# Performance work log

Hardware: AMD Instinct MI355X
Metric: run time of the kernel (lower is better)

The kernel has to match this reference:

```python
import jax, jax.numpy as jnp
import numpy as np

C = 32
C_Z = 128
S = 256   # MSA depth
N = 384   # residues


def setup_inputs() -> dict:
    key = jax.random.key(0)
    ks = jax.random.split(key, 7)
    m = jax.random.normal(ks[0], (S, N, C), dtype=jnp.float32)
    gamma = jnp.ones((C,), dtype=jnp.float32)
    beta = jnp.zeros((C,), dtype=jnp.float32)
    # projections stored as [in, out]
    W1 = jax.random.normal(ks[1], (C, C), dtype=jnp.float32) / np.sqrt(C)
    W2 = jax.random.normal(ks[2], (C, C), dtype=jnp.float32) / np.sqrt(C)
    W3 = jax.random.normal(ks[3], (C * C, C_Z), dtype=jnp.float32) / np.sqrt(C * C)
    b3 = jnp.zeros((C_Z,), dtype=jnp.float32)
    return {"m": m, "gamma": gamma, "beta": beta, "W1": W1, "W2": W2, "W3": W3, "b3": b3}


def reference(m, gamma, beta, W1, W2, W3, b3):
    # LayerNorm over channel dim
    mu = jnp.mean(m, axis=-1, keepdims=True)
    var = jnp.mean(jnp.square(m - mu), axis=-1, keepdims=True)
    mn = (m - mu) * jax.lax.rsqrt(var + 1e-5) * gamma + beta
    a = jnp.einsum('sic,cd->sid', mn, W1)  # [s, n, c]
    b = jnp.einsum('sic,cd->sid', mn, W2)  # [s, n, c]
    # outer product, mean over MSA dim s -> [n, n, c, c]
    o = jnp.einsum('sic,sjd->ijcd', a, b) / a.shape[0]
    o = o.reshape(o.shape[0], o.shape[1], C * C)  # [n, n, c*c]
    z = o @ W3 + b3  # [n, n, c_z]
    return z
```

## Files before the change

kernel.cpp:

```cpp
#include <hip/hip_runtime.h>

#define S_DEPTH 256
#define NRES 384
#define CIN 32
#define CZ 128
#define MDIM (NRES * CIN)

typedef short bf16x8 __attribute__((ext_vector_type(8)));
typedef short short4v __attribute__((ext_vector_type(4)));
typedef float f32x4 __attribute__((ext_vector_type(4)));

static __device__ __forceinline__ unsigned short f2bf(float f) {
  unsigned int u = __float_as_uint(f);
  unsigned int r = (u + 0x7fffu + ((u >> 16) & 1u)) >> 16;
  return (unsigned short)r;
}

static __device__ __forceinline__ void gld16(const void* g, void* l) {
  __builtin_amdgcn_global_load_lds((__attribute__((address_space(1))) void*)(g),
                                   (__attribute__((address_space(3))) void*)(l),
                                   16, 0, 0);
}

__global__ __launch_bounds__(256) void k_pre(
    const float* __restrict__ mm, const float* __restrict__ gamma,
    const float* __restrict__ beta, const float* __restrict__ W1,
    const float* __restrict__ W2, const float* __restrict__ W3,
    unsigned short* __restrict__ aT, unsigned short* __restrict__ bT,
    unsigned short* __restrict__ W3T) {
  __shared__ __align__(16) char sraw[256 * 33 * 4];
  const int t = threadIdx.x;

  if (blockIdx.x < 16) {
    unsigned short (*tile)[72] = (unsigned short(*)[72])sraw;
    const int b = blockIdx.x;
    const int d0 = (b & 7) * 4;
    const int e0 = (b >> 3) * 64;
#pragma unroll
    for (int iter = 0; iter < 32; ++iter) {
      int lr_ = iter * 4 + (t >> 6);
      int c = lr_ >> 2, dl = lr_ & 3;
      int q = c * 32 + d0 + dl;
      tile[lr_][t & 63] = f2bf(W3[q * 128 + e0 + (t & 63)]);
    }
    __syncthreads();
    const int e_l = t >> 2;
    const int dl = t & 3;
    unsigned short* dst = W3T + (((size_t)(d0 + dl) * 128) + e0 + e_l) * 32;
#pragma unroll
    for (int j = 0; j < 32; ++j) dst[j] = tile[j * 4 + dl][e_l];
    return;
  }

  float* buf = (float*)sraw;
  const int i = blockIdx.x - 16;

#pragma unroll
  for (int it = 0; it < 8; ++it) {
    int s = it * 32 + (t >> 3);
    int c4 = (t & 7) * 4;
    const float4 v = *(const float4*)(mm + ((size_t)s * NRES + i) * CIN + c4);
    buf[s * 33 + c4 + 0] = v.x;
    buf[s * 33 + c4 + 1] = v.y;
    buf[s * 33 + c4 + 2] = v.z;
    buf[s * 33 + c4 + 3] = v.w;
  }
  __syncthreads();

  float x[32];
#pragma unroll
  for (int k = 0; k < 32; ++k) x[k] = buf[t * 33 + k];
  float mu = 0.f;
#pragma unroll
  for (int k = 0; k < 32; ++k) mu += x[k];
  mu *= (1.f / 32.f);
  float var = 0.f;
#pragma unroll
  for (int k = 0; k < 32; ++k) {
    float dk = x[k] - mu;
    var += dk * dk;
  }
  var *= (1.f / 32.f);
  float inv = rsqrtf(var + 1e-5f);
#pragma unroll
  for (int k = 0; k < 32; ++k) x[k] = (x[k] - mu) * inv * gamma[k] + beta[k];

  float va[32], vb[32];
#pragma unroll
  for (int c = 0; c < 32; ++c) { va[c] = 0.f; vb[c] = 0.f; }
#pragma unroll
  for (int k = 0; k < 32; ++k) {
    float xk = x[k];
#pragma unroll
    for (int c = 0; c < 32; ++c) va[c] += xk * W1[k * 32 + c];
#pragma unroll
    for (int c = 0; c < 32; ++c) vb[c] += xk * W2[k * 32 + c];
  }

  unsigned short* dstA = aT + ((size_t)(t >> 6) * MDIM + (size_t)i * 32) * 64 + (t & 63);
  unsigned short* dstB = bT + ((size_t)(t >> 6) * MDIM + (size_t)i * 32) * 64 + (t & 63);
#pragma unroll
  for (int c = 0; c < 32; ++c) dstA[c * 64] = f2bf(va[c]);
#pragma unroll
  for (int c = 0; c < 32; ++c) dstB[c * 64] = f2bf(vb[c]);
}

__global__ __launch_bounds__(512, 2) void k_opm(
    const unsigned short* __restrict__ aT, const unsigned short* __restrict__ bT,
    const unsigned short* __restrict__ W3T, const float* __restrict__ b3,
    float* __restrict__ out) {
  __shared__ __align__(16) char smem[131072];
  const int t = threadIdx.x;
  const int w = t >> 6;
  const int l = t & 63;
  const int lr = l & 15;
  const int quad = l >> 4;
  const int wm = w >> 2, wn = w & 3;

  const int g = blockIdx.x;
  const int xcd = g & 7;
  const int rr = g >> 3;
  const int bx = rr / 6;
  const int by = xcd * 6 + (rr - bx * 6);
  const int m0 = by * 256;
  const int n0 = bx * 256;

  f32x4 acc[8][4];
#pragma unroll
  for (int mt = 0; mt < 8; ++mt)
#pragma unroll
    for (int nt = 0; nt < 4; ++nt) {
      acc[mt][nt][0] = 0.f; acc[mt][nt][1] = 0.f;
      acc[mt][nt][2] = 0.f; acc[mt][nt][3] = 0.f;
    }

  const int laneoff = (l >> 3) * 64 + (((l & 7) ^ (l >> 3)) * 8);
  const int r8 = lr & 7;

  {
    const unsigned short* aS = aT + (size_t)m0 * 64;
    const unsigned short* bS = bT + (size_t)n0 * 64;
#pragma unroll
    for (int p_ = 0; p_ < 4; ++p_) {
      int ch = p_ * 8 + w;
      gld16(aS + ch * 512 + laneoff, smem + ch * 1024);
      gld16(bS + ch * 512 + laneoff, smem + 32768 + ch * 1024);
    }
  }
  __syncthreads();

  for (int kt = 0; kt < 4; ++kt) {
    if (kt < 3) {
      char* nb = smem + ((kt + 1) & 1) * 65536;
      const unsigned short* aS = aT + ((size_t)(kt + 1) * MDIM + m0) * 64;
      const unsigned short* bS = bT + ((size_t)(kt + 1) * MDIM + n0) * 64;
#pragma unroll
      for (int p_ = 0; p_ < 4; ++p_) {
        int ch = p_ * 8 + w;
        gld16(aS + ch * 512 + laneoff, nb + ch * 1024);
        gld16(bS + ch * 512 + laneoff, nb + 32768 + ch * 1024);
      }
    }
    const char* cb = smem + (kt & 1) * 65536;
    const char* cbB = cb + 32768;

#pragma unroll
    for (int ks = 0; ks < 2; ++ks) {
      const int segoff = (((ks * 4 + quad) ^ r8) << 4);
      bf16x8 af[8];
#pragma unroll
      for (int mt = 0; mt < 8; ++mt) {
        int chunk = wm * 16 + mt * 2 + (lr >> 3);
        af[mt] = *(const bf16x8*)(cb + chunk * 1024 + r8 * 128 + segoff);
      }
#pragma unroll
      for (int nt = 0; nt < 4; ++nt) {
        int chunk = wn * 8 + nt * 2 + (lr >> 3);
        bf16x8 bfr = *(const bf16x8*)(cbB + chunk * 1024 + r8 * 128 + segoff);
#pragma unroll
        for (int mt = 0; mt < 8; ++mt)
          acc[mt][nt] =
              __builtin_amdgcn_mfma_f32_16x16x32_bf16(af[mt], bfr, acc[mt][nt], 0, 0, 0);
      }
    }
    __syncthreads();
  }

  const float scale = 1.0f / 256.0f;
#pragma unroll
  for (int mt = 0; mt < 8; ++mt) {
    int i_l = wm * 4 + (mt >> 1);
    int chc = 2 * (mt & 1) + (quad >> 1);
#pragma unroll
    for (int nt = 0; nt < 4; ++nt) {
      int j_l = wn * 2 + (nt >> 1);
      int d = (nt & 1) * 16 + lr;
      int p = i_l * 8 + j_l;
      int ch = d * 4 + chc;
      int key = (p ^ d) & 7;
      int off = p * 2048 + ((ch ^ key) << 4) + 8 * (quad & 1);
      short4v pk;
      pk[0] = (short)f2bf(acc[mt][nt][0] * scale);
      pk[1] = (short)f2bf(acc[mt][nt][1] * scale);
      pk[2] = (short)f2bf(acc[mt][nt][2] * scale);
      pk[3] = (short)f2bf(acc[mt][nt][3] * scale);
      *(short4v*)(smem + off) = pk;
    }
  }
  __syncthreads();

  f32x4 zacc[4];
#pragma unroll
  for (int a = 0; a < 4; ++a) {
    zacc[a][0] = 0.f; zacc[a][1] = 0.f; zacc[a][2] = 0.f; zacc[a][3] = 0.f;
  }
  const float bias = b3[w * 16 + lr];

  const unsigned short* wg = W3T + (size_t)(w * 16 + lr) * 32 + quad * 8;

  bf16x8 wcur = *(const bf16x8*)(wg);
#pragma unroll
  for (int kq = 0; kq < 32; ++kq) {
    bf16x8 wnxt;
    if (kq < 31) wnxt = *(const bf16x8*)(wg + (size_t)(kq + 1) * 4096);
    bf16x8 aef[4];
#pragma unroll
    for (int mte = 0; mte < 4; ++mte) {
      int row = mte * 16 + lr;
      int ch = kq * 4 + quad;
      int key = (row ^ kq) & 7;
      aef[mte] = *(const bf16x8*)(smem + row * 2048 + ((ch ^ key) << 4));
    }
#pragma unroll
    for (int mte = 0; mte < 4; ++mte)
      zacc[mte] = __builtin_amdgcn_mfma_f32_16x16x32_bf16(aef[mte], wcur, zacc[mte], 0, 0, 0);
    wcur = wnxt;
  }

  const int i0 = by * 8, j0 = bx * 8;
  const int e = w * 16 + lr;
#pragma unroll
  for (int mte = 0; mte < 4; ++mte)
#pragma unroll
    for (int r = 0; r < 4; ++r) {
      int p = mte * 16 + quad * 4 + r;
      out[(((size_t)(i0 + (p >> 3))) * NRES + (j0 + (p & 7))) * CZ + e] =
          zacc[mte][r] + bias;
    }
}

extern "C" void kernel_launch(void* const* d_in, const int* in_sizes, int n_in,
                              void* d_out, int out_size, void* d_ws, size_t ws_size,
                              hipStream_t stream) {
  const float* m = (const float*)d_in[0];
  const float* gamma = (const float*)d_in[1];
  const float* beta = (const float*)d_in[2];
  const float* W1 = (const float*)d_in[3];
  const float* W2 = (const float*)d_in[4];
  const float* W3 = (const float*)d_in[5];
  const float* b3 = (const float*)d_in[6];
  float* out = (float*)d_out;

  unsigned short* aT = (unsigned short*)d_ws;
  unsigned short* bT = aT + (size_t)MDIM * S_DEPTH;
  unsigned short* W3T = bT + (size_t)MDIM * S_DEPTH;

  k_pre<<<400, 256, 0, stream>>>(m, gamma, beta, W1, W2, W3, aT, bT, W3T);
  k_opm<<<2304, 512, 0, stream>>>(aT, bT, W3T, b3, out);
}
```

Measured before the change: 234.7 us.

## Split W3 projection across waves by K-quarter with LDS reduction

The second GEMM (o @ W3) used to give each wave 16 output channels over the full K=1024, so every wave read all 32 K-slices of the outer-product tile from LDS. Now each wave takes 64 output channels over one quarter of K. Each A fragment loaded from LDS feeds four MFMAs instead of one, which cuts LDS read traffic. The price is four times as many accumulator registers, an extra LDS write of the partial sums plus a 4-way reduction pass with two more barriers, and possible occupancy pressure under launch_bounds(512,2).

New measurement: 262.8 us. 11.9% more time.

```diff
diff --git a/kernel.cpp b/kernel.cpp
--- a/kernel.cpp
+++ b/kernel.cpp
@@ -209,20 +209,21 @@
   }
   __syncthreads();
 
-  f32x4 zacc[4];
-#pragma unroll
-  for (int a = 0; a < 4; ++a) {
-    zacc[a][0] = 0.f; zacc[a][1] = 0.f; zacc[a][2] = 0.f; zacc[a][3] = 0.f;
-  }
-  const float bias = b3[w * 16 + lr];
-
-  const unsigned short* wg = W3T + (size_t)(w * 16 + lr) * 32 + quad * 8;
-
-  bf16x8 wcur = *(const bf16x8*)(wg);
-#pragma unroll
-  for (int kq = 0; kq < 32; ++kq) {
-    bf16x8 wnxt;
-    if (kq < 31) wnxt = *(const bf16x8*)(wg + (size_t)(kq + 1) * 4096);
+  const int eh = w >> 2;
+  const int kh = w & 3;
+
+  f32x4 zacc[4][4];
+#pragma unroll
+  for (int a = 0; a < 4; ++a)
+#pragma unroll
+    for (int b_ = 0; b_ < 4; ++b_) {
+      zacc[a][b_][0] = 0.f; zacc[a][b_][1] = 0.f;
+      zacc[a][b_][2] = 0.f; zacc[a][b_][3] = 0.f;
+    }
+
+#pragma unroll
+  for (int kq8 = 0; kq8 < 8; ++kq8) {
+    const int kq = kh * 8 + kq8;
     bf16x8 aef[4];
 #pragma unroll
     for (int mte = 0; mte < 4; ++mte) {
@@ -232,21 +233,56 @@
       aef[mte] = *(const bf16x8*)(smem + row * 2048 + ((ch ^ key) << 4));
     }
 #pragma unroll
-    for (int mte = 0; mte < 4; ++mte)
-      zacc[mte] = __builtin_amdgcn_mfma_f32_16x16x32_bf16(aef[mte], wcur, zacc[mte], 0, 0, 0);
-    wcur = wnxt;
-  }
-
+    for (int ne = 0; ne < 4; ++ne) {
+      bf16x8 wf = *(const bf16x8*)(W3T + (size_t)kq * 4096 +
+                                   (size_t)(eh * 64 + ne * 16 + lr) * 32 + quad * 8);
+#pragma unroll
+      for (int mte = 0; mte < 4; ++mte)
+        zacc[mte][ne] =
+            __builtin_amdgcn_mfma_f32_16x16x32_bf16(aef[mte], wf, zacc[mte][ne], 0, 0, 0);
+    }
+  }
+
+  __syncthreads();
+  {
+    char* pb = smem + w * 16384;
+#pragma unroll
+    for (int mte = 0; mte < 4; ++mte) {
+      int p4 = mte * 16 + quad * 4;
+#pragma unroll
+      for (int ne = 0; ne < 4; ++ne) {
+        int ec = ne * 16 + lr;
+        int pw = p4 ^ ((ec & 7) << 3);
+        *(f32x4*)(pb + (ec * 64 + pw) * 4) = zacc[mte][ne];
+      }
+    }
+  }
+  __syncthreads();
+
+  const int eh2 = w >> 2;
+  const int rq = w & 3;
   const int i0 = by * 8, j0 = bx * 8;
-  const int e = w * 16 + lr;
-#pragma unroll
-  for (int mte = 0; mte < 4; ++mte)
+#pragma unroll
+  for (int ecg = 0; ecg < 4; ++ecg) {
+    int ec = ecg * 16 + lr;
+    int p4 = rq * 16 + quad * 4;
+    int pw = p4 ^ ((ec & 7) << 3);
+    size_t slot = (size_t)(ec * 64 + pw) * 4;
+    f32x4 sum = *(const f32x4*)(smem + (size_t)(eh2 * 4 + 0) * 16384 + slot);
+#pragma unroll
+    for (int kh2 = 1; kh2 < 4; ++kh2) {
+      f32x4 v = *(const f32x4*)(smem + (size_t)(eh2 * 4 + kh2) * 16384 + slot);
+      sum[0] += v[0]; sum[1] += v[1]; sum[2] += v[2]; sum[3] += v[3];
+    }
+    int e = eh2 * 64 + ec;
+    float bias = b3[e];
 #pragma unroll
     for (int r = 0; r < 4; ++r) {
-      int p = mte * 16 + quad * 4 + r;
+      int p = p4 + r;
       out[(((size_t)(i0 + (p >> 3))) * NRES + (j0 + (p & 7))) * CZ + e] =
-          zacc[mte][r] + bias;
-    }
+          sum[r] + bias;
+    }
+  }
 }
 
 extern "C" void kernel_launch(void* const* d_in, const int* in_sizes, int n_in,
```
